# Performance work log

Hardware: AMD Instinct MI355X
Metric: run time of the kernel (lower is better)

The kernel has to match this reference:

```python
import jax, jax.numpy as jnp
import numpy as np
from functools import partial

CONF_THR = 0.25
IOU_THR = 0.4
MAX_DET = 100
NMS_TOPK = 4096  # static candidate pool for JIT-safe NMS (>> MAX_DET)
N_ANCHORS = 120000
N_CLASSES = 80


def setup_inputs() -> dict:
    key = jax.random.key(0)
    k1, = jax.random.split(key, 1)
    # raw YOLOv5 head output: [1, N, 4(xywh) + 1(obj) + C(class probs)]
    prediction = jax.random.uniform(k1, (1, N_ANCHORS, 5 + N_CLASSES), dtype=jnp.float32)
    image_size = jnp.array([960, 1280], dtype=jnp.int64)  # original (h, w)
    input_size = jnp.array([480, 640], dtype=jnp.int64)   # network input (h, w)
    return {"prediction": prediction, "image_size": image_size, "input_size": input_size}


def _pairwise_iou(boxes):
    # boxes: [K, 4] xyxy -> [K, K] IoU
    x1, y1, x2, y2 = boxes[:, 0], boxes[:, 1], boxes[:, 2], boxes[:, 3]
    area = jnp.maximum(x2 - x1, 0.0) * jnp.maximum(y2 - y1, 0.0)
    ix1 = jnp.maximum(x1[:, None], x1[None, :])
    iy1 = jnp.maximum(y1[:, None], y1[None, :])
    ix2 = jnp.minimum(x2[:, None], x2[None, :])
    iy2 = jnp.minimum(y2[:, None], y2[None, :])
    inter = jnp.maximum(ix2 - ix1, 0.0) * jnp.maximum(iy2 - iy1, 0.0)
    union = area[:, None] + area[None, :] - inter
    return inter / jnp.maximum(union, 1e-9)


def _forward(prediction, image_size, input_size):
    det = prediction[0]                      # [N, 5+C]
    xy, wh = det[:, :2], det[:, 2:4]
    obj = det[:, 4]
    probs = det[:, 5:]                       # [N, C]
    clf = jnp.max(probs, axis=-1)
    labels = jnp.argmax(probs, axis=-1)
    scores = obj * clf
    boxes = jnp.concatenate([xy - wh * 0.5, xy + wh * 0.5], axis=-1)  # xywh -> xyxy

    valid = scores > CONF_THR
    masked_scores = jnp.where(valid, scores, -jnp.inf)
    # static top-K candidate pool, sorted by descending score (greedy NMS order)
    top_scores, top_idx = jax.lax.top_k(masked_scores, NMS_TOPK)
    cand_boxes = boxes[top_idx]              # [K, 4]
    cand_labels = labels[top_idx]
    cand_probs = probs[top_idx]              # [K, C]
    cand_valid = valid[top_idx]

    # class-batched NMS: offset boxes per class so boxes of different classes never overlap
    max_coord = jnp.max(jnp.where(cand_valid[:, None], cand_boxes, 0.0)) + 1.0
    off_boxes = cand_boxes + (cand_labels.astype(cand_boxes.dtype) * max_coord)[:, None]
    iou = _pairwise_iou(off_boxes)           # [K, K]

    K = NMS_TOPK
    idx = jnp.arange(K)

    def body(i, keep):
        suppress = keep[i] & (iou[i] > IOU_THR) & (idx > i)
        return keep & ~suppress

    keep = jax.lax.fori_loop(0, K, body, cand_valid)

    # take the MAX_DET highest-scoring kept boxes (candidates already score-sorted)
    sel_scores = jnp.where(keep, top_scores, -jnp.inf)
    fin_scores, fin_idx = jax.lax.top_k(sel_scores, MAX_DET)
    fin_valid = keep[fin_idx]
    fb = cand_boxes[fin_idx]                 # [MAX_DET, 4] xyxy, input-size coords
    fprobs = cand_probs[fin_idx]             # [MAX_DET, C]

    # rescale from input_size to image_size (undo letterbox), clip, then normalized xywh
    img = image_size.astype(fb.dtype)        # (h0, w0)
    inp = input_size.astype(fb.dtype)        # (h1, w1)
    gain = jnp.min(inp / img)
    pad = (inp - img * gain) * 0.5           # (pad_h, pad_w)
    x1 = jnp.clip((fb[:, 0] - pad[1]) / gain, 0.0, img[1])
    y1 = jnp.clip((fb[:, 1] - pad[0]) / gain, 0.0, img[0])
    x2 = jnp.clip((fb[:, 2] - pad[1]) / gain, 0.0, img[1])
    y2 = jnp.clip((fb[:, 3] - pad[0]) / gain, 0.0, img[0])
    h, w = img[0], img[1]
    out_boxes = jnp.stack([
        (x1 + x2) * 0.5 / w,
        (y1 + y2) * 0.5 / h,
        (x2 - x1) / w,
        (y2 - y1) / h,
    ], axis=-1)                               # [MAX_DET, 4]

    m = fin_valid.astype(out_boxes.dtype)[:, None]
    out_boxes = out_boxes * m                 # zero padded slots
    out_scores = jnp.where(fin_valid, fin_scores, 0.0)[:, None]
    out_probs = fprobs * m
    return out_boxes, out_scores, out_probs


def reference(prediction, image_size, input_size):
    return _forward(prediction, image_size, input_size)
```

## Files before the change

### kernel.cpp

```cpp
#include <hip/hip_runtime.h>
#include <math.h>

#define N_ANCH 120000
#define N_CLS  80
#define TOPK   4096
#define MAXDET 100
#define CONF   0.25f
#define IOUT   0.4f

__device__ __forceinline__ unsigned f2ord(float f) {
    unsigned u = __float_as_uint(f);
    return (u & 0x80000000u) ? ~u : (u | 0x80000000u);
}
__device__ __forceinline__ float ord2f(unsigned o) {
    unsigned u = (o & 0x80000000u) ? (o & 0x7FFFFFFFu) : ~o;
    return __uint_as_float(u);
}
__device__ __forceinline__ unsigned long long shflx64(unsigned long long v, int m) {
    unsigned lo = (unsigned)__shfl_xor((int)(unsigned)v, m, 64);
    unsigned hi = (unsigned)__shfl_xor((int)(unsigned)(v >> 32), m, 64);
    return ((unsigned long long)hi << 32) | lo;
}
#define ORD_NEGINF 0x007FFFFFu
#define BMAP(b) ((((b) & 0xFFu) << 8) | ((unsigned)(b) >> 8))

__global__ __launch_bounds__(1024) void k_zero(unsigned* hist, unsigned* meta) {
    int i = blockIdx.x * 1024 + threadIdx.x;
    if (i < 65536) hist[i] = 0u;
    if (i < 64) meta[i] = 0u;
}

__global__ __launch_bounds__(256) void k_decode(const float* __restrict__ pred,
                                                unsigned* __restrict__ ord,
                                                int* __restrict__ lab,
                                                float4* __restrict__ box,
                                                unsigned* __restrict__ hist) {
    int wv = threadIdx.x >> 6, lane = threadIdx.x & 63;
    int a = blockIdx.x * 4 + wv;
    if (a >= N_ANCH) return;
    const float* p = pred + (long)a * 85;
    float v0 = p[lane];
    float v1 = (lane < 21) ? p[64 + lane] : 0.f;
    unsigned long long k0 = 0ull, k1 = 0ull;
    if (lane >= 5)
        k0 = ((unsigned long long)__float_as_uint(v0) << 32) | (0xFFFFFFFFu - (unsigned)(lane - 5));
    if (lane < 21)
        k1 = ((unsigned long long)__float_as_uint(v1) << 32) | (0xFFFFFFFFu - (unsigned)(59 + lane));
    unsigned long long key = k0 > k1 ? k0 : k1;
#pragma unroll
    for (int off = 1; off < 64; off <<= 1) {
        unsigned long long o = shflx64(key, off);
        if (o > key) key = o;
    }
    float best = __uint_as_float((unsigned)(key >> 32));
    int bl = (int)(0xFFFFFFFFu - (unsigned)(key & 0xFFFFFFFFu));
    float x = __shfl(v0, 0, 64), y = __shfl(v0, 1, 64);
    float w = __shfl(v0, 2, 64), h = __shfl(v0, 3, 64);
    float obj = __shfl(v0, 4, 64);
    if (lane == 0) {
        float sc = obj * best;
        bool valid = sc > CONF;
        float m = valid ? sc : -INFINITY;
        float hw = w * 0.5f, hh = h * 0.5f;
        float4 b;
        b.x = x - hw; b.y = y - hh; b.z = x + hw; b.w = y + hh;
        unsigned o = f2ord(m);
        ord[a] = o;
        lab[a] = bl;
        box[a] = b;
        if (valid) atomicAdd(&hist[BMAP(o >> 16)], 1u);
    }
}

__global__ __launch_bounds__(1024) void k_unperm(const unsigned* __restrict__ hist,
                                                 unsigned* __restrict__ cnt,
                                                 unsigned* __restrict__ chunkSum) {
    int b = blockIdx.x * 1024 + threadIdx.x;
    unsigned v = hist[BMAP(b)];
    cnt[b] = v;
    unsigned s = v;
#pragma unroll
    for (int off = 1; off < 64; off <<= 1) s += (unsigned)__shfl_xor((int)s, off, 64);
    if ((threadIdx.x & 63) == 0) chunkSum[b >> 6] = s;
}

__global__ __launch_bounds__(1024) void k_select(unsigned* hist, const unsigned* __restrict__ cnt,
                                                 const unsigned* __restrict__ chunkSum,
                                                 unsigned* meta, int mode) {
    __shared__ unsigned part[1024];
    int t = threadIdx.x;
    unsigned target = (mode == 0) ? (unsigned)TOPK : meta[2];
    int base = t * 64;
    unsigned local;
    if (mode == 0) {
        local = chunkSum[t];
    } else {
        local = 0;
        for (int i = 0; i < 64; ++i) local += hist[base + i];
    }
    part[t] = local;
    __syncthreads();
    for (int off = 1; off < 1024; off <<= 1) {
        unsigned v = (t + off < 1024) ? part[t + off] : 0u;
        __syncthreads();
        part[t] += v;
        __syncthreads();
    }
    unsigned incl = part[t];
    unsigned after = (t + 1 < 1024) ? part[t + 1] : 0u;
    if (after < target && incl >= target) {
        const unsigned* src = (mode == 0) ? cnt : hist;
        unsigned c64[64];
#pragma unroll
        for (int i = 0; i < 64; ++i) c64[i] = src[base + i];
        unsigned run = after;
        for (int i = 63; i >= 0; --i) {
            unsigned c = c64[i];
            if (run + c >= target) {
                if (mode == 0) {
                    meta[0] = (unsigned)(base + i);
                    meta[1] = run;
                    meta[2] = (unsigned)TOPK - run;
                } else {
                    meta[3] = (meta[0] << 16) | (unsigned)(base + i);
                    meta[4] = meta[1] + run;
                    meta[5] = meta[2] - run;
                }
                break;
            }
            run += c;
        }
    }
    if (mode == 0) {
        for (int i = 0; i < 64; ++i) hist[base + i] = 0u;
        if (t == 0 && part[0] < target) {
            meta[0] = ORD_NEGINF >> 16;
            meta[1] = part[0];
            meta[2] = target - part[0];
        }
    }
}

__global__ __launch_bounds__(256) void k_hist2(const unsigned* __restrict__ ord,
                                               const unsigned* __restrict__ meta,
                                               unsigned* __restrict__ hist) {
    int a = blockIdx.x * 256 + threadIdx.x;
    if (a >= N_ANCH) return;
    unsigned o = ord[a];
    bool inBin = ((o >> 16) == meta[0]);
    bool isInv = inBin && (o == ORD_NEGINF);
    unsigned long long balInv = __ballot(isInv);
    if (inBin) {
        if (isInv) {
            int lane = threadIdx.x & 63;
            if (lane == __ffsll(balInv) - 1)
                atomicAdd(&hist[ORD_NEGINF & 0xFFFFu], (unsigned)__popcll(balInv));
        } else {
            atomicAdd(&hist[o & 0xFFFFu], 1u);
        }
    }
}

__global__ __launch_bounds__(256) void k_compact(const unsigned* __restrict__ ord,
                                                 unsigned* meta,
                                                 unsigned long long* __restrict__ keys,
                                                 unsigned* __restrict__ eq) {
    __shared__ unsigned wcGt[4], wcEq[4], sBaseGt, sBaseEq;
    int a = blockIdx.x * 256 + threadIdx.x;
    int lane = threadIdx.x & 63, wv = threadIdx.x >> 6;
    unsigned T = meta[3];
    unsigned o = (a < N_ANCH) ? ord[a] : 0u;
    bool isGt = (a < N_ANCH) && (o > T);
    bool isEq = (a < N_ANCH) && (o == T);
    unsigned long long balGt = __ballot(isGt);
    unsigned long long balEq = __ballot(isEq);
    if (lane == 0) {
        wcGt[wv] = (unsigned)__popcll(balGt);
        wcEq[wv] = (unsigned)__popcll(balEq);
    }
    __syncthreads();
    if (threadIdx.x == 0) {
        unsigned tg = wcGt[0] + wcGt[1] + wcGt[2] + wcGt[3];
        unsigned te = wcEq[0] + wcEq[1] + wcEq[2] + wcEq[3];
        sBaseGt = tg ? atomicAdd(&meta[6], tg) : 0u;
        sBaseEq = te ? atomicAdd(&meta[48], te) : 0u;
    }
    __syncthreads();
    unsigned long long ltmask = (lane == 63) ? ~0ull >> 1 : (1ull << lane) - 1ull;
    if (isGt) {
        unsigned p = sBaseGt;
        for (int w = 0; w < wv; ++w) p += wcGt[w];
        p += (unsigned)__popcll(balGt & ltmask);
        keys[p] = ((unsigned long long)o << 32) | (unsigned)(~(unsigned)a);
    } else if (isEq) {
        unsigned p = sBaseEq;
        for (int w = 0; w < wv; ++w) p += wcEq[w];
        p += (unsigned)__popcll(balEq & ltmask);
        if (p < TOPK) eq[p] = (unsigned)a;
    }
}

__global__ __launch_bounds__(1024) void k_eqsort(const unsigned* __restrict__ eq,
                                                 unsigned* meta,
                                                 unsigned long long* keys) {
    __shared__ unsigned s[TOPK];
    int t = threadIdx.x;
    unsigned n = meta[48]; if (n > TOPK) n = TOPK;
    unsigned remEq = meta[5];
    unsigned baseA = meta[4];
    unsigned T = meta[3];
    if (remEq == 0) return;
    if (n > remEq) {
        unsigned m = 1; while (m < n) m <<= 1;
        for (unsigned i = t; i < m; i += 1024) s[i] = (i < n) ? eq[i] : 0xFFFFFFFFu;
        __syncthreads();
        for (unsigned k = 2; k <= m; k <<= 1)
            for (unsigned j = k >> 1; j > 0; j >>= 1) {
                for (unsigned idx = t; idx < m; idx += 1024) {
                    unsigned ixj = idx ^ j;
                    if (ixj > idx) {
                        unsigned a = s[idx], b = s[ixj];
                        bool asc = ((idx & k) == 0);
                        bool sw = asc ? (a > b) : (a < b);
                        if (sw) { s[idx] = b; s[ixj] = a; }
                    }
                }
                __syncthreads();
            }
        for (unsigned r = t; r < remEq; r += 1024)
            keys[baseA + r] = ((unsigned long long)T << 32) | (unsigned)(~s[r]);
    } else {
        for (unsigned r = t; r < remEq; r += 1024)
            keys[baseA + r] = ((unsigned long long)T << 32) | (unsigned)(~eq[r]);
    }
}

__global__ __launch_bounds__(1024) void k_rank(const unsigned long long* __restrict__ keys,
                                               const int* __restrict__ lab,
                                               const float4* __restrict__ box,
                                               int* __restrict__ cIdx,
                                               float* __restrict__ cScore,
                                               int* __restrict__ cLab,
                                               float4* __restrict__ cBox,
                                               unsigned* meta) {
    __shared__ float smax[16];
    int wv = threadIdx.x >> 6, lane = threadIdx.x & 63;
    int i = blockIdx.x * 16 + wv;
    unsigned long long ki = keys[i];
    unsigned cnt = 0;
#pragma unroll 8
    for (int k = 0; k < 64; ++k)
        cnt += (keys[(k << 6) + lane] > ki) ? 1u : 0u;
#pragma unroll
    for (int off = 1; off < 64; off <<= 1) cnt += (unsigned)__shfl_xor((int)cnt, off, 64);
    if (lane == 0) {
        int r = (int)cnt;
        unsigned o = (unsigned)(ki >> 32);
        unsigned a = ~(unsigned)(ki & 0xFFFFFFFFu);
        float sc = ord2f(o);
        cIdx[r] = (int)a;
        cScore[r] = sc;
        cLab[r] = lab[a];
        float4 b = box[a];
        cBox[r] = b;
        float mx = 0.f;
        if (sc > CONF)
            mx = fmaxf(0.f, fmaxf(fmaxf(b.x, b.y), fmaxf(b.z, b.w)));
        smax[wv] = mx;
    }
    __syncthreads();
    if (threadIdx.x == 0) {
        float m = 0.f;
#pragma unroll
        for (int q = 0; q < 16; ++q) m = fmaxf(m, smax[q]);
        if (m > 0.f) atomicMax(&meta[8], __float_as_uint(m));
    }
}

__global__ __launch_bounds__(256) void k_mask(const float4* __restrict__ cBox,
                                              const int* __restrict__ cLab,
                                              const unsigned* __restrict__ meta,
                                              unsigned long long* __restrict__ M,
                                              unsigned long long* __restrict__ Diag) {
    int lane = threadIdx.x & 63;
    int i = blockIdx.x * 4 + (threadIdx.x >> 6);
    float mc = __uint_as_float(meta[8]) + 1.0f;
    float4 b = cBox[i];
    float offi = (float)cLab[i] * mc;
    float4 bi;
    bi.x = b.x + offi; bi.y = b.y + offi; bi.z = b.z + offi; bi.w = b.w + offi;
    float ai = fmaxf(bi.z - bi.x, 0.f) * fmaxf(bi.w - bi.y, 0.f);
    int w0 = i >> 6;
    unsigned long long myWord = 0ull;
    for (int jw = w0; jw < 64; ++jw) {
        int j = (jw << 6) + lane;
        float4 c = cBox[j];
        float offj = (float)cLab[j] * mc;
        float4 bj;
        bj.x = c.x + offj; bj.y = c.y + offj; bj.z = c.z + offj; bj.w = c.w + offj;
        float aj = fmaxf(bj.z - bj.x, 0.f) * fmaxf(bj.w - bj.y, 0.f);
        float ix1 = fmaxf(bi.x, bj.x), iy1 = fmaxf(bi.y, bj.y);
        float ix2 = fminf(bi.z, bj.z), iy2 = fminf(bi.w, bj.w);
        float inter = fmaxf(ix2 - ix1, 0.f) * fmaxf(iy2 - iy1, 0.f);
        float uni = ai + aj - inter;
        float iou = inter / fmaxf(uni, 1e-9f);
        bool bit = (j > i) & (iou > IOUT);
        unsigned long long word = __ballot(bit);
        if (lane == jw) myWord = word;
    }
    M[(long)i * 64 + lane] = myWord;
    if (lane == w0) Diag[i] = myWord;
}

__global__ __launch_bounds__(256) void k_nmsfinal(const unsigned long long* __restrict__ M,
                                                  const unsigned long long* __restrict__ Diag,
                                                  const float* __restrict__ cScore,
                                                  const float4* __restrict__ cBox,
                                                  const int* __restrict__ cIdx,
                                                  const float* __restrict__ pred,
                                                  const int* __restrict__ img,
                                                  const int* __restrict__ inp,
                                                  float* __restrict__ out,
                                                  int out_size) {
    __shared__ unsigned long long keepW[64];
    __shared__ int sel[MAXDET];
    __shared__ int nsel;
    int t = threadIdx.x;
    for (int i = t; i < out_size; i += 256) out[i] = 0.f;
    if (t == 0) nsel = 0;
    if (t < 64) {
        int lane = t;
        unsigned long long S = 0ull;
#pragma unroll 8
        for (int b = 0; b < 64; ++b) {
            float sc = cScore[(b << 6) + lane];
            unsigned long long bal = __ballot(!(sc > CONF));
            if (lane == b) S = bal;
        }
        unsigned long long d0 = Diag[lane];
        unsigned long long d1 = Diag[64 + lane];
        unsigned cnt = 0;
        int tstop = -1;
        unsigned long long ktStop = 0ull;
        for (int tt = 0; tt < 64; ++tt) {
            unsigned long long dcur = d0;
            d0 = d1;
            if (tt + 2 < 64) d1 = Diag[(tt + 2) * 64 + lane];
            unsigned long long s_tile =
                ((unsigned long long)(unsigned)__builtin_amdgcn_readlane((int)(unsigned)(S >> 32), tt)
                 << 32) |
                (unsigned)__builtin_amdgcn_readlane((int)(unsigned)S, tt);
#pragma unroll
            for (int b = 0; b < 64; ++b) {
                unsigned rl = (unsigned)__builtin_amdgcn_readlane((int)(unsigned)dcur, b);
                unsigned rh = (unsigned)__builtin_amdgcn_readlane((int)(unsigned)(dcur >> 32), b);
                unsigned long long row = ((unsigned long long)rh << 32) | rl;
                s_tile |= (((s_tile >> b) & 1ull) == 0ull) ? row : 0ull;
            }
            unsigned long long kt = ~s_tile;
            cnt += (unsigned)__popcll(kt);
            if (cnt >= MAXDET) { tstop = tt; ktStop = kt; break; }
            const unsigned long long* Mrow = M + (long)(tt << 6) * 64 + lane;
            unsigned long long a0 = 0, a1 = 0, a2 = 0, a3 = 0;
#pragma unroll
            for (int b = 0; b < 64; b += 4) {
                a0 |= Mrow[(long)(b + 0) * 64] & (0ull - ((kt >> (b + 0)) & 1ull));
                a1 |= Mrow[(long)(b + 1) * 64] & (0ull - ((kt >> (b + 1)) & 1ull));
                a2 |= Mrow[(long)(b + 2) * 64] & (0ull - ((kt >> (b + 2)) & 1ull));
                a3 |= Mrow[(long)(b + 3) * 64] & (0ull - ((kt >> (b + 3)) & 1ull));
            }
            S |= (a0 | a1) | (a2 | a3);
        }
        if (tstop >= 0) {
            keepW[lane] = (lane < tstop) ? ~S : (lane == tstop ? ktStop : 0ull);
        } else {
            keepW[lane] = ~S;
        }
    }
    __syncthreads();
    if (t < 64) {
        unsigned long long kw = keepW[t];
        int cnt = __popcll(kw);
        int incl = cnt;
        for (int off = 1; off < 64; off <<= 1) {
            int v = __shfl_up(incl, off);
            if (t >= off) incl += v;
        }
        int rk = incl - cnt;
        if (t == 63) nsel = (incl < MAXDET) ? incl : MAXDET;
        unsigned long long m = kw;
        while (m) {
            int b = __ffsll((unsigned long long)m) - 1;
            m &= m - 1;
            if (rk < MAXDET) sel[rk] = (t << 6) + b;
            ++rk;
        }
    }
    __syncthreads();
    int nk = nsel;
    int ih_i = img[0], iw_i = img[1];
    int nh_i = inp[0], nw_i = inp[1];
    if (iw_i == 0) iw_i = img[2];
    if (nw_i == 0) nw_i = inp[2];
    float ih = (float)ih_i, iw = (float)iw_i;
    float nh = (float)nh_i, nw = (float)nw_i;
    float gain = fminf(nh / ih, nw / iw);
    float pad0 = (nh - ih * gain) * 0.5f;
    float pad1 = (nw - iw * gain) * 0.5f;
    for (int o = t; o < nk; o += 256) {
        int k = sel[o];
        float4 b = cBox[k];
        float x1 = fminf(fmaxf((b.x - pad1) / gain, 0.f), iw);
        float y1 = fminf(fmaxf((b.y - pad0) / gain, 0.f), ih);
        float x2 = fminf(fmaxf((b.z - pad1) / gain, 0.f), iw);
        float y2 = fminf(fmaxf((b.w - pad0) / gain, 0.f), ih);
        out[o * 4 + 0] = (x1 + x2) * 0.5f / iw;
        out[o * 4 + 1] = (y1 + y2) * 0.5f / ih;
        out[o * 4 + 2] = (x2 - x1) / iw;
        out[o * 4 + 3] = (y2 - y1) / ih;
        out[4 * MAXDET + o] = cScore[k];
    }
    for (int p = t; p < nk * N_CLS; p += 256) {
        int o = p / N_CLS, c = p - o * N_CLS;
        int a = cIdx[sel[o]];
        out[5 * MAXDET + p] = pred[(long)a * 85 + 5 + c];
    }
}

extern "C" void kernel_launch(void* const* d_in, const int* in_sizes, int n_in,
                              void* d_out, int out_size, void* d_ws, size_t ws_size,
                              hipStream_t stream) {
    const float* pred = (const float*)d_in[0];
    const int* img = (const int*)d_in[1];
    const int* inp = (const int*)d_in[2];
    float* out = (float*)d_out;
    unsigned char* W = (unsigned char*)d_ws;

    unsigned* hist                = (unsigned*)(W + 0);
    unsigned* meta                = (unsigned*)(W + 262144);
    unsigned* ord                 = (unsigned*)(W + 262400);
    int* lab                      = (int*)(W + 742400);
    float4* box                   = (float4*)(W + 1222400);
    unsigned long long* keys      = (unsigned long long*)(W + 3142400);
    unsigned* eq                  = (unsigned*)(W + 3175168);
    int* cIdx                     = (int*)(W + 3191552);
    float* cScore                 = (float*)(W + 3207936);
    int* cLab                     = (int*)(W + 3224320);
    float4* cBox                  = (float4*)(W + 3240704);
    unsigned long long* M         = (unsigned long long*)(W + 3388160);
    unsigned long long* Diag      = (unsigned long long*)(W + 262400);
    unsigned* cnt_lin             = (unsigned*)(W + 3388160);
    unsigned* chunkSum            = (unsigned*)(W + 3650304);

    int nb = (N_ANCH + 255) / 256;
    int nwb = (N_ANCH + 3) / 4;
    k_zero<<<64, 1024, 0, stream>>>(hist, meta);
    k_decode<<<nwb, 256, 0, stream>>>(pred, ord, lab, box, hist);
    k_unperm<<<64, 1024, 0, stream>>>(hist, cnt_lin, chunkSum);
    k_select<<<1, 1024, 0, stream>>>(hist, cnt_lin, chunkSum, meta, 0);
    k_hist2<<<nb, 256, 0, stream>>>(ord, meta, hist);
    k_select<<<1, 1024, 0, stream>>>(hist, cnt_lin, chunkSum, meta, 1);
    k_compact<<<nb, 256, 0, stream>>>(ord, meta, keys, eq);
    k_eqsort<<<1, 1024, 0, stream>>>(eq, meta, keys);
    k_rank<<<256, 1024, 0, stream>>>(keys, lab, box, cIdx, cScore, cLab, cBox, meta);
    k_mask<<<1024, 256, 0, stream>>>(cBox, cLab, meta, M, Diag);
    k_nmsfinal<<<1, 256, 0, stream>>>(M, Diag, cScore, cBox, cIdx, pred, img, inp, out, out_size);
}
```

Measured before the change: 123.1 us.

## Replace two-pass radix select with one-pass bin select and rank over superset

Drops the second histogram pass, the second select launch and the tie-index bitonic sort. Every anchor whose top 16 key bits reach the boundary bin is now compacted into a key buffer capped at KEYCAP. k_rank then counts how many keys beat each one across the whole candidate set and keeps those ranked below TOPK. This cuts three launches but makes the rank step quadratic in the superset size. It also risks losing candidates if the boundary bin pushes the count past the cap.

```diff
diff --git a/kernel.cpp b/kernel.cpp
--- a/kernel.cpp
+++ b/kernel.cpp
@@ -7,6 +7,7 @@
 #define MAXDET 100
 #define CONF   0.25f
 #define IOUT   0.4f
+#define KEYCAP 30720
 
 __device__ __forceinline__ unsigned f2ord(float f) {
     unsigned u = __float_as_uint(f);
@@ -84,21 +85,12 @@
     if ((threadIdx.x & 63) == 0) chunkSum[b >> 6] = s;
 }
 
-__global__ __launch_bounds__(1024) void k_select(unsigned* hist, const unsigned* __restrict__ cnt,
-                                                 const unsigned* __restrict__ chunkSum,
-                                                 unsigned* meta, int mode) {
+__global__ __launch_bounds__(1024) void k_select0(const unsigned* __restrict__ cnt,
+                                                  const unsigned* __restrict__ chunkSum,
+                                                  unsigned* meta) {
     __shared__ unsigned part[1024];
     int t = threadIdx.x;
-    unsigned target = (mode == 0) ? (unsigned)TOPK : meta[2];
-    int base = t * 64;
-    unsigned local;
-    if (mode == 0) {
-        local = chunkSum[t];
-    } else {
-        local = 0;
-        for (int i = 0; i < 64; ++i) local += hist[base + i];
-    }
-    part[t] = local;
+    part[t] = chunkSum[t];
     __syncthreads();
     for (int off = 1; off < 1024; off <<= 1) {
         unsigned v = (t + off < 1024) ? part[t + off] : 0u;
@@ -108,130 +100,44 @@
     }
     unsigned incl = part[t];
     unsigned after = (t + 1 < 1024) ? part[t + 1] : 0u;
-    if (after < target && incl >= target) {
-        const unsigned* src = (mode == 0) ? cnt : hist;
+    if (after < (unsigned)TOPK && incl >= (unsigned)TOPK) {
+        int base = t * 64;
         unsigned c64[64];
 #pragma unroll
-        for (int i = 0; i < 64; ++i) c64[i] = src[base + i];
+        for (int i = 0; i < 64; ++i) c64[i] = cnt[base + i];
         unsigned run = after;
         for (int i = 63; i >= 0; --i) {
             unsigned c = c64[i];
-            if (run + c >= target) {
-                if (mode == 0) {
-                    meta[0] = (unsigned)(base + i);
-                    meta[1] = run;
-                    meta[2] = (unsigned)TOPK - run;
-                } else {
-                    meta[3] = (meta[0] << 16) | (unsigned)(base + i);
-                    meta[4] = meta[1] + run;
-                    meta[5] = meta[2] - run;
-                }
-                break;
-            }
+            if (run + c >= (unsigned)TOPK) { meta[0] = (unsigned)(base + i); break; }
             run += c;
-        }
-    }
-    if (mode == 0) {
-        for (int i = 0; i < 64; ++i) hist[base + i] = 0u;
-        if (t == 0 && part[0] < target) {
-            meta[0] = ORD_NEGINF >> 16;
-            meta[1] = part[0];
-            meta[2] = target - part[0];
-        }
-    }
-}
-
-__global__ __launch_bounds__(256) void k_hist2(const unsigned* __restrict__ ord,
-                                               const unsigned* __restrict__ meta,
-                                               unsigned* __restrict__ hist) {
-    int a = blockIdx.x * 256 + threadIdx.x;
-    if (a >= N_ANCH) return;
-    unsigned o = ord[a];
-    bool inBin = ((o >> 16) == meta[0]);
-    bool isInv = inBin && (o == ORD_NEGINF);
-    unsigned long long balInv = __ballot(isInv);
-    if (inBin) {
-        if (isInv) {
-            int lane = threadIdx.x & 63;
-            if (lane == __ffsll(balInv) - 1)
-                atomicAdd(&hist[ORD_NEGINF & 0xFFFFu], (unsigned)__popcll(balInv));
-        } else {
-            atomicAdd(&hist[o & 0xFFFFu], 1u);
         }
     }
 }
 
 __global__ __launch_bounds__(256) void k_compact(const unsigned* __restrict__ ord,
                                                  unsigned* meta,
-                                                 unsigned long long* __restrict__ keys,
-                                                 unsigned* __restrict__ eq) {
-    __shared__ unsigned wcGt[4], wcEq[4], sBaseGt, sBaseEq;
+                                                 unsigned long long* __restrict__ keys) {
+    __shared__ unsigned wc[4];
+    __shared__ unsigned sBase;
     int a = blockIdx.x * 256 + threadIdx.x;
     int lane = threadIdx.x & 63, wv = threadIdx.x >> 6;
-    unsigned T = meta[3];
+    unsigned b1 = meta[0];
     unsigned o = (a < N_ANCH) ? ord[a] : 0u;
-    bool isGt = (a < N_ANCH) && (o > T);
-    bool isEq = (a < N_ANCH) && (o == T);
-    unsigned long long balGt = __ballot(isGt);
-    unsigned long long balEq = __ballot(isEq);
-    if (lane == 0) {
-        wcGt[wv] = (unsigned)__popcll(balGt);
-        wcEq[wv] = (unsigned)__popcll(balEq);
-    }
+    bool isC = (a < N_ANCH) && ((o >> 16) >= b1);
+    unsigned long long bal = __ballot(isC);
+    if (lane == 0) wc[wv] = (unsigned)__popcll(bal);
     __syncthreads();
     if (threadIdx.x == 0) {
-        unsigned tg = wcGt[0] + wcGt[1] + wcGt[2] + wcGt[3];
-        unsigned te = wcEq[0] + wcEq[1] + wcEq[2] + wcEq[3];
-        sBaseGt = tg ? atomicAdd(&meta[6], tg) : 0u;
-        sBaseEq = te ? atomicAdd(&meta[48], te) : 0u;
+        unsigned tg = wc[0] + wc[1] + wc[2] + wc[3];
+        sBase = tg ? atomicAdd(&meta[6], tg) : 0u;
     }
     __syncthreads();
     unsigned long long ltmask = (lane == 63) ? ~0ull >> 1 : (1ull << lane) - 1ull;
-    if (isGt) {
-        unsigned p = sBaseGt;
-        for (int w = 0; w < wv; ++w) p += wcGt[w];
-        p += (unsigned)__popcll(balGt & ltmask);
-        keys[p] = ((unsigned long long)o << 32) | (unsigned)(~(unsigned)a);
-    } else if (isEq) {
-        unsigned p = sBaseEq;
-        for (int w = 0; w < wv; ++w) p += wcEq[w];
-        p += (unsigned)__popcll(balEq & ltmask);
-        if (p < TOPK) eq[p] = (unsigned)a;
-    }
-}
-
-__global__ __launch_bounds__(1024) void k_eqsort(const unsigned* __restrict__ eq,
-                                                 unsigned* meta,
-                                                 unsigned long long* keys) {
-    __shared__ unsigned s[TOPK];
-    int t = threadIdx.x;
-    unsigned n = meta[48]; if (n > TOPK) n = TOPK;
-    unsigned remEq = meta[5];
-    unsigned baseA = meta[4];
-    unsigned T = meta[3];
-    if (remEq == 0) return;
-    if (n > remEq) {
-        unsigned m = 1; while (m < n) m <<= 1;
-        for (unsigned i = t; i < m; i += 1024) s[i] = (i < n) ? eq[i] : 0xFFFFFFFFu;
-        __syncthreads();
-        for (unsigned k = 2; k <= m; k <<= 1)
-            for (unsigned j = k >> 1; j > 0; j >>= 1) {
-                for (unsigned idx = t; idx < m; idx += 1024) {
-                    unsigned ixj = idx ^ j;
-                    if (ixj > idx) {
-                        unsigned a = s[idx], b = s[ixj];
-                        bool asc = ((idx & k) == 0);
-                        bool sw = asc ? (a > b) : (a < b);
-                        if (sw) { s[idx] = b; s[ixj] = a; }
-                    }
-                }
-                __syncthreads();
-            }
-        for (unsigned r = t; r < remEq; r += 1024)
-            keys[baseA + r] = ((unsigned long long)T << 32) | (unsigned)(~s[r]);
-    } else {
-        for (unsigned r = t; r < remEq; r += 1024)
-            keys[baseA + r] = ((unsigned long long)T << 32) | (unsigned)(~eq[r]);
+    if (isC) {
+        unsigned p = sBase;
+        for (int w = 0; w < wv; ++w) p += wc[w];
+        p += (unsigned)__popcll(bal & ltmask);
+        if (p < KEYCAP) keys[p] = ((unsigned long long)o << 32) | (unsigned)(~(unsigned)a);
     }
 }
 
@@ -245,29 +151,36 @@
                                                unsigned* meta) {
     __shared__ float smax[16];
     int wv = threadIdx.x >> 6, lane = threadIdx.x & 63;
-    int i = blockIdx.x * 16 + wv;
-    unsigned long long ki = keys[i];
-    unsigned cnt = 0;
+    unsigned K = meta[6];
+    if (K > KEYCAP) K = KEYCAP;
+    int nw = (int)((K + 63) >> 6);
+    float mymax = 0.f;
+    for (int i = blockIdx.x * 16 + wv; i < (int)K; i += 256 * 16) {
+        unsigned long long ki = keys[i];
+        unsigned cnt = 0;
 #pragma unroll 8
-    for (int k = 0; k < 64; ++k)
-        cnt += (keys[(k << 6) + lane] > ki) ? 1u : 0u;
-#pragma unroll
-    for (int off = 1; off < 64; off <<= 1) cnt += (unsigned)__shfl_xor((int)cnt, off, 64);
-    if (lane == 0) {
-        int r = (int)cnt;
-        unsigned o = (unsigned)(ki >> 32);
-        unsigned a = ~(unsigned)(ki & 0xFFFFFFFFu);
-        float sc = ord2f(o);
-        cIdx[r] = (int)a;
-        cScore[r] = sc;
-        cLab[r] = lab[a];
-        float4 b = box[a];
-        cBox[r] = b;
-        float mx = 0.f;
-        if (sc > CONF)
-            mx = fmaxf(0.f, fmaxf(fmaxf(b.x, b.y), fmaxf(b.z, b.w)));
-        smax[wv] = mx;
-    }
+        for (int k = 0; k < nw; ++k) {
+            int idx = (k << 6) + lane;
+            unsigned long long kv = (idx < (int)K) ? keys[idx] : 0ull;
+            cnt += (kv > ki) ? 1u : 0u;
+        }
+#pragma unroll
+        for (int off = 1; off < 64; off <<= 1) cnt += (unsigned)__shfl_xor((int)cnt, off, 64);
+        if (lane == 0 && cnt < (unsigned)TOPK) {
+            int r = (int)cnt;
+            unsigned o = (unsigned)(ki >> 32);
+            unsigned a = ~(unsigned)(ki & 0xFFFFFFFFu);
+            float sc = ord2f(o);
+            cIdx[r] = (int)a;
+            cScore[r] = sc;
+            cLab[r] = lab[a];
+            float4 b = box[a];
+            cBox[r] = b;
+            if (sc > CONF)
+                mymax = fmaxf(mymax, fmaxf(0.f, fmaxf(fmaxf(b.x, b.y), fmaxf(b.z, b.w))));
+        }
+    }
+    if (lane == 0) smax[wv] = mymax;
     __syncthreads();
     if (threadIdx.x == 0) {
         float m = 0.f;
@@ -442,13 +355,12 @@
     int* lab                      = (int*)(W + 742400);
     float4* box                   = (float4*)(W + 1222400);
     unsigned long long* keys      = (unsigned long long*)(W + 3142400);
-    unsigned* eq                  = (unsigned*)(W + 3175168);
-    int* cIdx                     = (int*)(W + 3191552);
-    float* cScore                 = (float*)(W + 3207936);
-    int* cLab                     = (int*)(W + 3224320);
-    float4* cBox                  = (float4*)(W + 3240704);
     unsigned long long* M         = (unsigned long long*)(W + 3388160);
     unsigned long long* Diag      = (unsigned long long*)(W + 262400);
+    int* cIdx                     = (int*)(W + 295168);
+    float* cScore                 = (float*)(W + 311552);
+    int* cLab                     = (int*)(W + 327936);
+    float4* cBox                  = (float4*)(W + 344320);
     unsigned* cnt_lin             = (unsigned*)(W + 3388160);
     unsigned* chunkSum            = (unsigned*)(W + 3650304);
 
@@ -457,11 +369,8 @@
     k_zero<<<64, 1024, 0, stream>>>(hist, meta);
     k_decode<<<nwb, 256, 0, stream>>>(pred, ord, lab, box, hist);
     k_unperm<<<64, 1024, 0, stream>>>(hist, cnt_lin, chunkSum);
-    k_select<<<1, 1024, 0, stream>>>(hist, cnt_lin, chunkSum, meta, 0);
-    k_hist2<<<nb, 256, 0, stream>>>(ord, meta, hist);
-    k_select<<<1, 1024, 0, stream>>>(hist, cnt_lin, chunkSum, meta, 1);
-    k_compact<<<nb, 256, 0, stream>>>(ord, meta, keys, eq);
-    k_eqsort<<<1, 1024, 0, stream>>>(eq, meta, keys);
+    k_select0<<<1, 1024, 0, stream>>>(cnt_lin, chunkSum, meta);
+    k_compact<<<nb, 256, 0, stream>>>(ord, meta, keys);
     k_rank<<<256, 1024, 0, stream>>>(keys, lab, box, cIdx, cScore, cLab, cBox, meta);
     k_mask<<<1024, 256, 0, stream>>>(cBox, cLab, meta, M, Diag);
     k_nmsfinal<<<1, 256, 0, stream>>>(M, Diag, cScore, cBox, cIdx, pred, img, inp, out, out_size);
```

New measurement: 115.9 us. 5.8% less time.
